# Kernel tuning notes

Measured on AMD Instinct MI355X. Metric: run time of the kernel, lower is better.

The kernel has to match this reference:

```python
import jax, jax.numpy as jnp
import numpy as np

N_ATOMS = 100_000
N_EDGES = 1_600_000
N_RADIAL = 16
N_ELEM = 119          # periodic table size used by per-element scale/shift
HIDDEN = 512
N_FEAT = N_RADIAL + N_RADIAL * N_RADIAL  # M0 + M1-contraction features = 272
R_CUT = 5.0
EPS = 1e-8


def setup_inputs() -> dict:
    key = jax.random.key(0)
    ks = jax.random.split(key, 10)
    R = jax.random.normal(ks[0], (N_ATOMS, 3), jnp.float32)
    Z = jax.random.randint(ks[1], (N_ATOMS,), 0, N_ELEM).astype(jnp.int32)
    idx = jax.random.randint(ks[2], (2, N_EDGES), 0, N_ATOMS)
    box = jnp.zeros((3, 3), jnp.float32)
    offsets = jnp.zeros((N_EDGES, 3), jnp.float32)
    # descriptor params: Gaussian radial basis centers / width
    centers = jnp.linspace(0.0, R_CUT, N_RADIAL, dtype=jnp.float32)
    width = jnp.asarray(0.5, jnp.float32)
    # readout MLP params
    W1 = jax.random.normal(ks[3], (N_FEAT, HIDDEN), jnp.float32) / np.sqrt(N_FEAT)
    b1 = jnp.zeros((HIDDEN,), jnp.float32)
    W2 = jax.random.normal(ks[4], (HIDDEN, HIDDEN), jnp.float32) / np.sqrt(HIDDEN)
    b2 = jnp.zeros((HIDDEN,), jnp.float32)
    W3 = jax.random.normal(ks[5], (HIDDEN, 1), jnp.float32) / np.sqrt(HIDDEN)
    b3 = jnp.zeros((1,), jnp.float32)
    # per-element scale/shift
    scale = jnp.ones((N_ELEM,), jnp.float32)
    shift = jax.random.normal(ks[6], (N_ELEM,), jnp.float32)
    return {"R": R, "Z": Z, "idx": idx, "box": box, "offsets": offsets,
            "centers": centers, "width": width,
            "W1": W1, "b1": b1, "W2": W2, "b2": b2, "W3": W3, "b3": b3,
            "scale": scale, "shift": shift}


def reference(R, Z, idx, box, offsets, centers, width,
              W1, b1, W2, b2, W3, b3, scale, shift):
    n = R.shape[0]
    idx_i, idx_j = idx[0], idx[1]
    # edge gather + free displacement (init_box == 0): dr = displacement(Rj, Ri) = Rj - Ri
    dr = R[idx_j] - R[idx_i]                      # (E, 3)
    r = jnp.linalg.norm(dr, axis=-1, keepdims=True)  # (E, 1)
    d = dr / (r + EPS)                            # unit directions (E, 3)
    # Gaussian radial basis (E, K)
    b = jnp.exp(-((r - centers[None, :]) ** 2) / (2.0 * width * width))
    # scatter-sum moments per atom
    M0 = jax.ops.segment_sum(b, idx_i, num_segments=n)                       # (N, K)
    M1 = jax.ops.segment_sum(b[:, :, None] * d[:, None, :], idx_i,
                             num_segments=n)                                 # (N, K, 3)
    # rotation-invariant gaussian-moment contraction
    G1 = jnp.einsum('nad,nbd->nab', M1, M1).reshape(n, -1)                   # (N, K*K)
    feat = jnp.concatenate([M0, G1], axis=-1)                                # (N, 272)
    # per-atom readout MLP (swish)
    h = jax.nn.silu(feat @ W1 + b1)
    h = jax.nn.silu(h @ W2 + b2)
    h = h @ W3 + b3                                                          # (N, 1)
    # per-element scale/shift, then total energy
    atomic_energies = scale[Z][:, None] * h + shift[Z][:, None]
    return jnp.sum(atomic_energies)
```

## Files before the change

kernel.cpp:

```cpp
#include <hip/hip_runtime.h>
#include <hip/hip_bf16.h>
#include <cstdint>

#define HID 512
#define K1P 288

typedef __attribute__((ext_vector_type(8))) short bf16x8;
typedef __attribute__((ext_vector_type(4))) float f32x4;

__device__ __forceinline__ short f2bf(float x) {
    __hip_bfloat16 h = __float2bfloat16(x);
    return *(short*)&h;
}
__device__ __forceinline__ float silu(float x) {
    return x * (1.0f / (1.0f + __expf(-x)));
}
__device__ __forceinline__ void gl_lds16(const void* src, void* dst) {
    __builtin_amdgcn_global_load_lds(
        (const __attribute__((address_space(1))) void*)src,
        (__attribute__((address_space(3))) void*)dst, 16, 0, 0);
}
__device__ __forceinline__ int xcd_swz(int bid, int nwg) {
    int q = nwg >> 3, r = nwg & 7;
    int xcd = bid & 7, i = bid >> 3;
    int base = (xcd < r) ? xcd * (q + 1) : r * (q + 1) + (xcd - r) * q;
    return base + i;
}

__global__ __launch_bounds__(256) void hist_kernel(
    const int* __restrict__ idx, int* __restrict__ counts, int nEdges)
{
    int e = blockIdx.x * 256 + threadIdx.x;
    if (e < nEdges) atomicAdd(&counts[idx[e]], 1);
}

__global__ __launch_bounds__(1024) void scan1_kernel(
    const int* __restrict__ counts, int* __restrict__ starts,
    int* __restrict__ blockSum, int n)
{
    __shared__ int wsum[16];
    int t = threadIdx.x, lane = t & 63, wid = t >> 6;
    int i = blockIdx.x * 1024 + t;
    int v = (i < n) ? counts[i] : 0;
    int incl = v;
    #pragma unroll
    for (int off = 1; off < 64; off <<= 1) {
        int u = __shfl_up(incl, off);
        if (lane >= off) incl += u;
    }
    if (lane == 63) wsum[wid] = incl;
    __syncthreads();
    if (t < 16) {
        int s = wsum[t];
        #pragma unroll
        for (int off = 1; off < 16; off <<= 1) {
            int u = __shfl_up(s, off);
            if (t >= off) s += u;
        }
        wsum[t] = s;
    }
    __syncthreads();
    int woff = (wid == 0) ? 0 : wsum[wid - 1];
    if (i < n) starts[i] = woff + incl - v;
    if (t == 0) blockSum[blockIdx.x] = wsum[15];
}

__global__ __launch_bounds__(1024) void scan2_kernel(
    const int* __restrict__ blockSum, int* __restrict__ blockOff,
    int* __restrict__ starts, int nb, int n)
{
    __shared__ int arr[1024];
    int t = threadIdx.x;
    int v = (t < nb) ? blockSum[t] : 0;
    arr[t] = v;
    __syncthreads();
    #pragma unroll
    for (int off = 1; off < 1024; off <<= 1) {
        int x = (t >= off) ? arr[t - off] : 0;
        __syncthreads();
        arr[t] += x;
        __syncthreads();
    }
    if (t < nb) blockOff[t] = arr[t] - v;
    if (t == 0) starts[n] = arr[nb - 1];
}

__global__ __launch_bounds__(1024) void scan3_kernel(
    int* __restrict__ starts, int* __restrict__ cursor,
    const int* __restrict__ blockOff, int n)
{
    int i = blockIdx.x * 1024 + threadIdx.x;
    if (i < n) {
        int s = starts[i] + blockOff[blockIdx.x];
        starts[i] = s;
        cursor[i] = s;
    }
}

__global__ __launch_bounds__(256) void scatter_kernel(
    const float* __restrict__ R, const int* __restrict__ idx,
    int* __restrict__ cursor, float4* __restrict__ sorted, int nEdges)
{
    int e = blockIdx.x * 256 + threadIdx.x;
    if (e >= nEdges) return;
    int i = idx[e];
    int j = idx[nEdges + e];
    float rix = R[3*(size_t)i], riy = R[3*(size_t)i+1], riz = R[3*(size_t)i+2];
    float rjx = R[3*(size_t)j], rjy = R[3*(size_t)j+1], rjz = R[3*(size_t)j+2];
    float dx = rjx - rix, dy = rjy - riy, dz = rjz - riz;
    float r = sqrtf(dx*dx + dy*dy + dz*dz);
    float inv = 1.0f / (r + 1e-8f);
    int pos = atomicAdd(&cursor[i], 1);
    sorted[pos] = make_float4(r, dx*inv, dy*inv, dz*inv);
}

__global__ __launch_bounds__(256) void accum_kernel(
    const float4* __restrict__ sorted, const int* __restrict__ starts,
    const float* __restrict__ centers, const float* __restrict__ width,
    float* __restrict__ M0M1, short* __restrict__ feat16,
    int nAtoms, int useFeat)
{
    __shared__ float sm[4][64];
    int wv = threadIdx.x >> 6, lane = threadIdx.x & 63;
    int atom = blockIdx.x * 4 + wv;
    if (atom >= nAtoms) return;
    int s = starts[atom], e = starts[atom + 1];
    int k = lane >> 2, c = lane & 3;
    float ck = centers[k];
    float w = width[0];
    float inv2w2 = 1.0f / (2.0f * w * w);
    float acc = 0.0f;
    auto term = [&](float4 v) {
        float diff = v.x - ck;
        float b = __expf(-diff * diff * inv2w2);
        float comp = (c == 0) ? 1.0f : ((c == 1) ? v.y : ((c == 2) ? v.z : v.w));
        return b * comp;
    };
    int p = s;
    for (; p + 3 < e; p += 4) {
        float4 v0 = sorted[p];
        float4 v1 = sorted[p + 1];
        float4 v2 = sorted[p + 2];
        float4 v3 = sorted[p + 3];
        acc += term(v0); acc += term(v1); acc += term(v2); acc += term(v3);
    }
    for (; p < e; ++p) acc += term(sorted[p]);

    if (!useFeat) {
        M0M1[(size_t)atom * 64 + lane] = acc;
        return;
    }
    sm[wv][lane] = acc;
    asm volatile("s_waitcnt lgkmcnt(0)" ::: "memory");
    short* frow = feat16 + (size_t)atom * K1P;
    #pragma unroll
    for (int q = 0; q < 5; ++q) {
        int idx5 = q * 64 + lane;
        if (idx5 >= K1P) break;
        float val;
        if (idx5 < 16) {
            val = sm[wv][4 * idx5];
        } else if (idx5 < 272) {
            int g = idx5 - 16, a = g >> 4, b = g & 15;
            val = sm[wv][4*a+1] * sm[wv][4*b+1]
                + sm[wv][4*a+2] * sm[wv][4*b+2]
                + sm[wv][4*a+3] * sm[wv][4*b+3];
        } else {
            val = 0.0f;
        }
        frow[idx5] = f2bf(val);
    }
}

__global__ __launch_bounds__(256) void convW_kernel(
    const float* __restrict__ W, short* __restrict__ Wt, int K, int Kpad, int N)
{
    int n = blockIdx.x * 256 + threadIdx.x;
    int k = blockIdx.y;
    if (n >= N) return;
    float v = (k < K) ? W[(size_t)k * N + n] : 0.0f;
    Wt[(size_t)n * Kpad + k] = f2bf(v);
}

__global__ __launch_bounds__(256, 2) void gemm1_mfma(
    const float* __restrict__ M0M1, const short* __restrict__ W1t,
    const float* __restrict__ bias, short* __restrict__ C, int M, int nwg)
{
    __shared__ float MsT[64][128];
    __shared__ short Asl[2][4096];
    __shared__ short Bsl[4][4096];
    int t = threadIdx.x;
    int w = t >> 6, lane = t & 63;
    int wr = w >> 1, wc = w & 1;
    int li = lane & 15, lg = lane >> 4;
    int lin = xcd_swz(blockIdx.x, nwg);
    int row0 = (lin >> 2) * 128;
    int col0 = (lin & 3) * 128;

    {
        int mrow = t >> 1, mo = (t & 1) * 32;
        int gm = row0 + mrow; if (gm > M - 1) gm = M - 1;
        const float4* src = (const float4*)(M0M1 + (size_t)gm * 64 + mo);
        #pragma unroll
        for (int q = 0; q < 8; ++q) {
            float4 v = src[q];
            int c0 = mo + q * 4;
            MsT[c0+0][mrow] = v.x; MsT[c0+1][mrow] = v.y;
            MsT[c0+2][mrow] = v.z; MsT[c0+3][mrow] = v.w;
        }
    }
    __syncthreads();

    auto stageA = [&](int kt, int buf) {
        #pragma unroll
        for (int p = 0; p < 2; ++p) {
            int cell = p * 256 + t;
            int k8 = cell >> 7, row = cell & 127;
            int kbase = kt * 32 + k8 * 8;
            bf16x8 v;
            if (kbase < 16) {
                #pragma unroll
                for (int j = 0; j < 8; ++j) v[j] = f2bf(MsT[4*(kbase+j)][row]);
            } else if (kbase < 272) {
                int g = kbase - 16, a = g >> 4, b0 = g & 15;
                float ax = MsT[4*a+1][row], ay = MsT[4*a+2][row], az = MsT[4*a+3][row];
                #pragma unroll
                for (int j = 0; j < 8; ++j) {
                    int b = b0 + j;
                    v[j] = f2bf(ax*MsT[4*b+1][row] + ay*MsT[4*b+2][row] + az*MsT[4*b+3][row]);
                }
            } else {
                #pragma unroll
                for (int j = 0; j < 8; ++j) v[j] = 0;
            }
            *(bf16x8*)&Asl[buf][cell * 8] = v;
        }
    };
    auto stageB = [&](int kt, int buf) {
        #pragma unroll
        for (int p = 0; p < 2; ++p) {
            int cell = p * 256 + t;
            int k8 = cell >> 7, col = cell & 127;
            const short* src = W1t + (size_t)(col0 + col) * K1P + kt*32 + k8*8;
            gl_lds16(src, &Bsl[buf][(p * 256 + w * 64) * 8]);
        }
    };

    f32x4 acc[4][4] = {};
    const int NS = K1P / 32;
    stageA(0, 0);
    stageB(0, 0); stageB(1, 1); stageB(2, 2);

    #pragma unroll
    for (int s = 0; s < NS; ++s) {
        if (s <= NS - 3)      asm volatile("s_waitcnt vmcnt(4) lgkmcnt(0)\n\ts_barrier" ::: "memory");
        else if (s == NS - 2) asm volatile("s_waitcnt vmcnt(2) lgkmcnt(0)\n\ts_barrier" ::: "memory");
        else                  asm volatile("s_waitcnt vmcnt(0) lgkmcnt(0)\n\ts_barrier" ::: "memory");
        if (s + 3 < NS) stageB(s + 3, (s + 3) & 3);
        bf16x8 af[4], bfr[4];
        #pragma unroll
        for (int m = 0; m < 4; ++m)
            af[m] = *(const bf16x8*)&Asl[s & 1][(lg*128 + wr*64 + m*16 + li) * 8];
        #pragma unroll
        for (int n = 0; n < 4; ++n)
            bfr[n] = *(const bf16x8*)&Bsl[s & 3][(lg*128 + wc*64 + n*16 + li) * 8];
        if (s + 1 < NS) stageA(s + 1, (s + 1) & 1);
        __builtin_amdgcn_s_setprio(1);
        #pragma unroll
        for (int m = 0; m < 4; ++m)
            #pragma unroll
            for (int n = 0; n < 4; ++n)
                acc[m][n] = __builtin_amdgcn_mfma_f32_16x16x32_bf16(af[m], bfr[n], acc[m][n], 0, 0, 0);
        __builtin_amdgcn_s_setprio(0);
    }

    float bv[4];
    #pragma unroll
    for (int n = 0; n < 4; ++n) bv[n] = bias[col0 + wc*64 + n*16 + li];
    #pragma unroll
    for (int m = 0; m < 4; ++m)
        #pragma unroll
        for (int r = 0; r < 4; ++r) {
            int row = row0 + wr*64 + m*16 + lg*4 + r;
            if (row >= M) continue;
            size_t base = (size_t)row * HID + col0 + wc*64 + li;
            #pragma unroll
            for (int n = 0; n < 4; ++n) {
                float cx = acc[m][n][r] + bv[n];
                C[base + n*16] = f2bf(silu(cx));
            }
        }
}

__global__ __launch_bounds__(256, 3) void gemm_feat(
    const short* __restrict__ F, const short* __restrict__ W1t,
    const float* __restrict__ bias, short* __restrict__ C, int M, int nwg)
{
    __shared__ short Asl[3][4096];
    __shared__ short Bsl[3][4096];
    int t = threadIdx.x;
    int w = t >> 6, lane = t & 63;
    int wr = w >> 1, wc = w & 1;
    int li = lane & 15, lg = lane >> 4;
    int lin = xcd_swz(blockIdx.x, nwg);
    int row0 = (lin >> 2) * 128;
    int col0 = (lin & 3) * 128;

    int rr = t & 127, k8h = t >> 7;
    int grA = row0 + rr; if (grA > M - 1) grA = M - 1;
    const short* aSrc0 = F + (size_t)grA * K1P + k8h * 8;
    const short* aSrc1 = aSrc0 + 16;
    const short* bSrc0 = W1t + (size_t)(col0 + rr) * K1P + k8h * 8;
    const short* bSrc1 = bSrc0 + 16;

    auto stage = [&](int kt, int buf) {
        gl_lds16(aSrc0 + kt * 32, &Asl[buf][(w * 64) * 8]);
        gl_lds16(aSrc1 + kt * 32, &Asl[buf][(256 + w * 64) * 8]);
        gl_lds16(bSrc0 + kt * 32, &Bsl[buf][(w * 64) * 8]);
        gl_lds16(bSrc1 + kt * 32, &Bsl[buf][(256 + w * 64) * 8]);
    };

    f32x4 acc[4][4] = {};
    const int NS = K1P / 32;
    stage(0, 0); stage(1, 1);

    #pragma unroll
    for (int s = 0; s < NS; ++s) {
        if (s < NS - 1) asm volatile("s_waitcnt vmcnt(4)\n\ts_barrier" ::: "memory");
        else            asm volatile("s_waitcnt vmcnt(0)\n\ts_barrier" ::: "memory");
        if (s + 2 < NS) stage(s + 2, (s + 2) % 3);
        bf16x8 af[4], bfr[4];
        #pragma unroll
        for (int m = 0; m < 4; ++m)
            af[m] = *(const bf16x8*)&Asl[s % 3][(lg*128 + wr*64 + m*16 + li) * 8];
        #pragma unroll
        for (int n = 0; n < 4; ++n)
            bfr[n] = *(const bf16x8*)&Bsl[s % 3][(lg*128 + wc*64 + n*16 + li) * 8];
        __builtin_amdgcn_s_setprio(1);
        #pragma unroll
        for (int m = 0; m < 4; ++m)
            #pragma unroll
            for (int n = 0; n < 4; ++n)
                acc[m][n] = __builtin_amdgcn_mfma_f32_16x16x32_bf16(af[m], bfr[n], acc[m][n], 0, 0, 0);
        __builtin_amdgcn_s_setprio(0);
    }

    float bv[4];
    #pragma unroll
    for (int n = 0; n < 4; ++n) bv[n] = bias[col0 + wc*64 + n*16 + li];
    #pragma unroll
    for (int m = 0; m < 4; ++m)
        #pragma unroll
        for (int r = 0; r < 4; ++r) {
            int row = row0 + wr*64 + m*16 + lg*4 + r;
            if (row >= M) continue;
            size_t base = (size_t)row * HID + col0 + wc*64 + li;
            #pragma unroll
            for (int n = 0; n < 4; ++n) {
                float cx = acc[m][n][r] + bv[n];
                C[base + n*16] = f2bf(silu(cx));
            }
        }
}

__global__ __launch_bounds__(256, 3) void gemm2_mfma(
    const short* __restrict__ A, const short* __restrict__ W2t,
    const float* __restrict__ bias, const float* __restrict__ W3,
    const float* __restrict__ b3, const float* __restrict__ scale,
    const float* __restrict__ shift, const int* __restrict__ Z,
    float* __restrict__ out, int M, int nwg)
{
    __shared__ short Asl[3][4096];
    __shared__ short Bsl[3][4096];
    __shared__ float rsum[2][128];
    __shared__ float red[4];
    int t = threadIdx.x;
    int w = t >> 6, lane = t & 63;
    int wr = w >> 1, wc = w & 1;
    int li = lane & 15, lg = lane >> 4;
    int lin = xcd_swz(blockIdx.x, nwg);
    int row0 = (lin >> 2) * 128;
    int col0 = (lin & 3) * 128;

    int rr = t & 127, k8h = t >> 7;
    int grA = row0 + rr; if (grA > M - 1) grA = M - 1;
    const short* aSrc0 = A + (size_t)grA * HID + k8h * 8;
    const short* aSrc1 = aSrc0 + 16;
    const short* bSrc0 = W2t + (size_t)(col0 + rr) * HID + k8h * 8;
    const short* bSrc1 = bSrc0 + 16;

    auto stage = [&](int kt, int buf) {
        gl_lds16(aSrc0 + kt * 32, &Asl[buf][(w * 64) * 8]);
        gl_lds16(aSrc1 + kt * 32, &Asl[buf][(256 + w * 64) * 8]);
        gl_lds16(bSrc0 + kt * 32, &Bsl[buf][(w * 64) * 8]);
        gl_lds16(bSrc1 + kt * 32, &Bsl[buf][(256 + w * 64) * 8]);
    };

    f32x4 acc[4][4] = {};
    const int NS = HID / 32;
    stage(0, 0); stage(1, 1);

    for (int s = 0; s < NS; ++s) {
        if (s < NS - 1) asm volatile("s_waitcnt vmcnt(4)\n\ts_barrier" ::: "memory");
        else            asm volatile("s_waitcnt vmcnt(0)\n\ts_barrier" ::: "memory");
        if (s + 2 < NS) stage(s + 2, (s + 2) % 3);
        bf16x8 af[4], bfr[4];
        #pragma unroll
        for (int m = 0; m < 4; ++m)
            af[m] = *(const bf16x8*)&Asl[s % 3][(lg*128 + wr*64 + m*16 + li) * 8];
        #pragma unroll
        for (int n = 0; n < 4; ++n)
            bfr[n] = *(const bf16x8*)&Bsl[s % 3][(lg*128 + wc*64 + n*16 + li) * 8];
        __builtin_amdgcn_s_setprio(1);
        #pragma unroll
        for (int m = 0; m < 4; ++m)
            #pragma unroll
            for (int n = 0; n < 4; ++n)
                acc[m][n] = __builtin_amdgcn_mfma_f32_16x16x32_bf16(af[m], bfr[n], acc[m][n], 0, 0, 0);
        __builtin_amdgcn_s_setprio(0);
    }

    float bv[4], w3v[4];
    #pragma unroll
    for (int n = 0; n < 4; ++n) {
        int col = col0 + wc*64 + n*16 + li;
        bv[n]  = bias[col];
        w3v[n] = W3[col];
    }
    #pragma unroll
    for (int m = 0; m < 4; ++m)
        #pragma unroll
        for (int r = 0; r < 4; ++r) {
            float s = 0.f;
            #pragma unroll
            for (int n = 0; n < 4; ++n) {
                float cx = acc[m][n][r] + bv[n];
                s += silu(cx) * w3v[n];
            }
            #pragma unroll
            for (int off = 1; off < 16; off <<= 1) s += __shfl_xor(s, off);
            if (li == 0) rsum[wc][wr*64 + m*16 + lg*4 + r] = s;
        }
    __syncthreads();
    float e = 0.f;
    if (t < 128) {
        int row = row0 + t;
        if (row < M) {
            float v = rsum[0][t] + rsum[1][t];
            int z = Z[row];
            e = scale[z] * v;
            if ((lin & 3) == 0) e += scale[z] * b3[0] + shift[z];
        }
    }
    #pragma unroll
    for (int off = 32; off > 0; off >>= 1) e += __shfl_down(e, off);
    if (lane == 0) red[w] = e;
    __syncthreads();
    if (t == 0) atomicAdd(out, red[0] + red[1] + red[2] + red[3]);
}

extern "C" void kernel_launch(void* const* d_in, const int* in_sizes, int n_in,
                              void* d_out, int out_size, void* d_ws, size_t ws_size,
                              hipStream_t stream)
{
    const float* R       = (const float*)d_in[0];
    const int*   Z       = (const int*)  d_in[1];
    const int*   idx     = (const int*)  d_in[2];
    const float* centers = (const float*)d_in[5];
    const float* width   = (const float*)d_in[6];
    const float* W1      = (const float*)d_in[7];
    const float* b1      = (const float*)d_in[8];
    const float* W2      = (const float*)d_in[9];
    const float* b2      = (const float*)d_in[10];
    const float* W3      = (const float*)d_in[11];
    const float* b3      = (const float*)d_in[12];
    const float* scale   = (const float*)d_in[13];
    const float* shift   = (const float*)d_in[14];

    int nAtoms = in_sizes[0] / 3;
    int nEdges = in_sizes[2] / 2;

    size_t m0m1_b = (size_t)nAtoms * 64 * sizeof(float);
    size_t h1_b   = (size_t)nAtoms * HID * 2;
    size_t w1t_b  = (size_t)HID * K1P * 2;
    size_t w2t_b  = (size_t)HID * HID * 2;
    size_t feat_b = (size_t)nAtoms * K1P * 2;
    if (ws_size < m0m1_b + h1_b + w1t_b + w2t_b) return;
    int useFeat = (ws_size >= m0m1_b + h1_b + w1t_b + w2t_b + feat_b) ? 1 : 0;

    char* ws = (char*)d_ws;
    float* M0M1  = (float*)ws;
    char*  regB  = ws + m0m1_b;
    short* h1    = (short*)regB;
    short* W1t   = (short*)(ws + m0m1_b + h1_b);
    short* W2t   = W1t + (size_t)HID * K1P;
    short* feat16 = (short*)(ws + m0m1_b + h1_b + w1t_b + w2t_b);

    int nb = (nAtoms + 1023) / 1024;
    size_t sorted_b = (size_t)nEdges * sizeof(float4);
    float4* sorted = (float4*)regB;
    int* counts   = (int*)(regB + sorted_b);
    int* starts   = counts + nAtoms;
    int* cursor   = starts + nAtoms + 1;
    int* blockSum = cursor + nAtoms;
    int* blockOff = blockSum + nb;
    if (sorted_b + (size_t)(3 * nAtoms + 1 + 2 * nb) * sizeof(int) > h1_b) return;

    float* out = (float*)d_out;

    hipMemsetAsync(counts, 0, (size_t)nAtoms * sizeof(int), stream);
    hipMemsetAsync(out, 0, sizeof(float), stream);

    convW_kernel<<<dim3(2, K1P), 256, 0, stream>>>(W1, W1t, 272, K1P, HID);
    convW_kernel<<<dim3(2, HID), 256, 0, stream>>>(W2, W2t, HID, HID, HID);

    int eb = (nEdges + 255) / 256;
    hist_kernel <<<eb, 256, 0, stream>>>(idx, counts, nEdges);
    scan1_kernel<<<nb, 1024, 0, stream>>>(counts, starts, blockSum, nAtoms);
    scan2_kernel<<<1, 1024, 0, stream>>>(blockSum, blockOff, starts, nb, nAtoms);
    scan3_kernel<<<nb, 1024, 0, stream>>>(starts, cursor, blockOff, nAtoms);
    scatter_kernel<<<eb, 256, 0, stream>>>(R, idx, cursor, sorted, nEdges);
    accum_kernel<<<(nAtoms + 3) / 4, 256, 0, stream>>>(sorted, starts, centers, width,
                                                       M0M1, feat16, nAtoms, useFeat);

    int gb = (nAtoms + 127) / 128;
    int nwg = gb * 4;
    if (useFeat)
        gemm_feat<<<nwg, 256, 0, stream>>>(feat16, W1t, b1, h1, nAtoms, nwg);
    else
        gemm1_mfma<<<nwg, 256, 0, stream>>>(M0M1, W1t, b1, h1, nAtoms, nwg);
    gemm2_mfma<<<nwg, 256, 0, stream>>>(h1, W2t, b2, W3, b3, scale, shift, Z, out, nAtoms, nwg);
}
```

Measured before the change: 435.9 us.

## Widen GEMM tiles to 128x256 with 512-thread blocks for MLP layers

Both MLP GEMM kernels now use 512-thread blocks (8 waves in a 2x4 layout) that each compute a 128x256 output tile instead of 128x128. Each A tile is loaded once per block and reused across twice as many output columns, which halves A-side global/LDS traffic and halves the number of workgroups. The cost is more LDS per block, fewer blocks resident per CU, and fewer blocks overall, which may reduce occupancy and latency hiding. The final reduction in the second GEMM is widened to four column groups.

```diff
diff --git a/kernel.cpp b/kernel.cpp
--- a/kernel.cpp
+++ b/kernel.cpp
@@ -292,32 +292,34 @@
         }
 }
 
-__global__ __launch_bounds__(256, 3) void gemm_feat(
+__global__ __launch_bounds__(512) void gemm_feat(
     const short* __restrict__ F, const short* __restrict__ W1t,
     const float* __restrict__ bias, short* __restrict__ C, int M, int nwg)
 {
     __shared__ short Asl[3][4096];
-    __shared__ short Bsl[3][4096];
+    __shared__ short Bsl[3][8192];
     int t = threadIdx.x;
     int w = t >> 6, lane = t & 63;
-    int wr = w >> 1, wc = w & 1;
+    int wr = w >> 2, wc = w & 3;
     int li = lane & 15, lg = lane >> 4;
     int lin = xcd_swz(blockIdx.x, nwg);
-    int row0 = (lin >> 2) * 128;
-    int col0 = (lin & 3) * 128;
-
-    int rr = t & 127, k8h = t >> 7;
-    int grA = row0 + rr; if (grA > M - 1) grA = M - 1;
-    const short* aSrc0 = F + (size_t)grA * K1P + k8h * 8;
-    const short* aSrc1 = aSrc0 + 16;
-    const short* bSrc0 = W1t + (size_t)(col0 + rr) * K1P + k8h * 8;
-    const short* bSrc1 = bSrc0 + 16;
+    int row0 = (lin >> 1) * 128;
+    int colB = (lin & 1) * 256;
+
+    int k8A = t >> 7, rowA = t & 127;
+    int grA = row0 + rowA; if (grA > M - 1) grA = M - 1;
+    const short* aSrc = F + (size_t)grA * K1P + k8A * 8;
+    int cellB = t;
+    int k8B0 = cellB >> 8, colB0 = cellB & 255;
+    const short* bSrc0 = W1t + (size_t)(colB + colB0) * K1P + k8B0 * 8;
+    int cellB1 = 512 + t;
+    int k8B1 = cellB1 >> 8, colB1 = cellB1 & 255;
+    const short* bSrc1 = W1t + (size_t)(colB + colB1) * K1P + k8B1 * 8;
 
     auto stage = [&](int kt, int buf) {
-        gl_lds16(aSrc0 + kt * 32, &Asl[buf][(w * 64) * 8]);
-        gl_lds16(aSrc1 + kt * 32, &Asl[buf][(256 + w * 64) * 8]);
+        gl_lds16(aSrc + kt * 32, &Asl[buf][(w * 64) * 8]);
         gl_lds16(bSrc0 + kt * 32, &Bsl[buf][(w * 64) * 8]);
-        gl_lds16(bSrc1 + kt * 32, &Bsl[buf][(256 + w * 64) * 8]);
+        gl_lds16(bSrc1 + kt * 32, &Bsl[buf][(512 + w * 64) * 8]);
     };
 
     f32x4 acc[4][4] = {};
@@ -326,7 +328,7 @@
 
     #pragma unroll
     for (int s = 0; s < NS; ++s) {
-        if (s < NS - 1) asm volatile("s_waitcnt vmcnt(4)\n\ts_barrier" ::: "memory");
+        if (s < NS - 1) asm volatile("s_waitcnt vmcnt(3)\n\ts_barrier" ::: "memory");
         else            asm volatile("s_waitcnt vmcnt(0)\n\ts_barrier" ::: "memory");
         if (s + 2 < NS) stage(s + 2, (s + 2) % 3);
         bf16x8 af[4], bfr[4];
@@ -335,7 +337,7 @@
             af[m] = *(const bf16x8*)&Asl[s % 3][(lg*128 + wr*64 + m*16 + li) * 8];
         #pragma unroll
         for (int n = 0; n < 4; ++n)
-            bfr[n] = *(const bf16x8*)&Bsl[s % 3][(lg*128 + wc*64 + n*16 + li) * 8];
+            bfr[n] = *(const bf16x8*)&Bsl[s % 3][(lg*256 + wc*64 + n*16 + li) * 8];
         __builtin_amdgcn_s_setprio(1);
         #pragma unroll
         for (int m = 0; m < 4; ++m)
@@ -347,14 +349,14 @@
 
     float bv[4];
     #pragma unroll
-    for (int n = 0; n < 4; ++n) bv[n] = bias[col0 + wc*64 + n*16 + li];
+    for (int n = 0; n < 4; ++n) bv[n] = bias[colB + wc*64 + n*16 + li];
     #pragma unroll
     for (int m = 0; m < 4; ++m)
         #pragma unroll
         for (int r = 0; r < 4; ++r) {
             int row = row0 + wr*64 + m*16 + lg*4 + r;
             if (row >= M) continue;
-            size_t base = (size_t)row * HID + col0 + wc*64 + li;
+            size_t base = (size_t)row * HID + colB + wc*64 + li;
             #pragma unroll
             for (int n = 0; n < 4; ++n) {
                 float cx = acc[m][n][r] + bv[n];
@@ -363,7 +365,7 @@
         }
 }
 
-__global__ __launch_bounds__(256, 3) void gemm2_mfma(
+__global__ __launch_bounds__(512) void gemm2_mfma(
     const short* __restrict__ A, const short* __restrict__ W2t,
     const float* __restrict__ bias, const float* __restrict__ W3,
     const float* __restrict__ b3, const float* __restrict__ scale,
@@ -371,29 +373,31 @@
     float* __restrict__ out, int M, int nwg)
 {
     __shared__ short Asl[3][4096];
-    __shared__ short Bsl[3][4096];
-    __shared__ float rsum[2][128];
-    __shared__ float red[4];
+    __shared__ short Bsl[3][8192];
+    __shared__ float rsum[4][128];
+    __shared__ float red[8];
     int t = threadIdx.x;
     int w = t >> 6, lane = t & 63;
-    int wr = w >> 1, wc = w & 1;
+    int wr = w >> 2, wc = w & 3;
     int li = lane & 15, lg = lane >> 4;
     int lin = xcd_swz(blockIdx.x, nwg);
-    int row0 = (lin >> 2) * 128;
-    int col0 = (lin & 3) * 128;
-
-    int rr = t & 127, k8h = t >> 7;
-    int grA = row0 + rr; if (grA > M - 1) grA = M - 1;
-    const short* aSrc0 = A + (size_t)grA * HID + k8h * 8;
-    const short* aSrc1 = aSrc0 + 16;
-    const short* bSrc0 = W2t + (size_t)(col0 + rr) * HID + k8h * 8;
-    const short* bSrc1 = bSrc0 + 16;
+    int row0 = (lin >> 1) * 128;
+    int colB = (lin & 1) * 256;
+
+    int k8A = t >> 7, rowA = t & 127;
+    int grA = row0 + rowA; if (grA > M - 1) grA = M - 1;
+    const short* aSrc = A + (size_t)grA * HID + k8A * 8;
+    int cellB = t;
+    int k8B0 = cellB >> 8, colB0 = cellB & 255;
+    const short* bSrc0 = W2t + (size_t)(colB + colB0) * HID + k8B0 * 8;
+    int cellB1 = 512 + t;
+    int k8B1 = cellB1 >> 8, colB1 = cellB1 & 255;
+    const short* bSrc1 = W2t + (size_t)(colB + colB1) * HID + k8B1 * 8;
 
     auto stage = [&](int kt, int buf) {
-        gl_lds16(aSrc0 + kt * 32, &Asl[buf][(w * 64) * 8]);
-        gl_lds16(aSrc1 + kt * 32, &Asl[buf][(256 + w * 64) * 8]);
+        gl_lds16(aSrc + kt * 32, &Asl[buf][(w * 64) * 8]);
         gl_lds16(bSrc0 + kt * 32, &Bsl[buf][(w * 64) * 8]);
-        gl_lds16(bSrc1 + kt * 32, &Bsl[buf][(256 + w * 64) * 8]);
+        gl_lds16(bSrc1 + kt * 32, &Bsl[buf][(512 + w * 64) * 8]);
     };
 
     f32x4 acc[4][4] = {};
@@ -401,7 +405,7 @@
     stage(0, 0); stage(1, 1);
 
     for (int s = 0; s < NS; ++s) {
-        if (s < NS - 1) asm volatile("s_waitcnt vmcnt(4)\n\ts_barrier" ::: "memory");
+        if (s < NS - 1) asm volatile("s_waitcnt vmcnt(3)\n\ts_barrier" ::: "memory");
         else            asm volatile("s_waitcnt vmcnt(0)\n\ts_barrier" ::: "memory");
         if (s + 2 < NS) stage(s + 2, (s + 2) % 3);
         bf16x8 af[4], bfr[4];
@@ -410,7 +414,7 @@
             af[m] = *(const bf16x8*)&Asl[s % 3][(lg*128 + wr*64 + m*16 + li) * 8];
         #pragma unroll
         for (int n = 0; n < 4; ++n)
-            bfr[n] = *(const bf16x8*)&Bsl[s % 3][(lg*128 + wc*64 + n*16 + li) * 8];
+            bfr[n] = *(const bf16x8*)&Bsl[s % 3][(lg*256 + wc*64 + n*16 + li) * 8];
         __builtin_amdgcn_s_setprio(1);
         #pragma unroll
         for (int m = 0; m < 4; ++m)
@@ -423,7 +427,7 @@
     float bv[4], w3v[4];
     #pragma unroll
     for (int n = 0; n < 4; ++n) {
-        int col = col0 + wc*64 + n*16 + li;
+        int col = colB + wc*64 + n*16 + li;
         bv[n]  = bias[col];
         w3v[n] = W3[col];
     }
@@ -446,17 +450,20 @@
     if (t < 128) {
         int row = row0 + t;
         if (row < M) {
-            float v = rsum[0][t] + rsum[1][t];
+            float v = rsum[0][t] + rsum[1][t] + rsum[2][t] + rsum[3][t];
             int z = Z[row];
             e = scale[z] * v;
-            if ((lin & 3) == 0) e += scale[z] * b3[0] + shift[z];
+            if ((lin & 1) == 0) e += scale[z] * b3[0] + shift[z];
         }
     }
     #pragma unroll
     for (int off = 32; off > 0; off >>= 1) e += __shfl_down(e, off);
     if (lane == 0) red[w] = e;
     __syncthreads();
-    if (t == 0) atomicAdd(out, red[0] + red[1] + red[2] + red[3]);
+    if (t == 0) {
+        float s2 = red[0] + red[1] + red[2] + red[3] + red[4] + red[5] + red[6] + red[7];
+        atomicAdd(out, s2);
+    }
 }
 
 extern "C" void kernel_launch(void* const* d_in, const int* in_sizes, int n_in,
@@ -524,10 +531,14 @@
                                                        M0M1, feat16, nAtoms, useFeat);
 
     int gb = (nAtoms + 127) / 128;
-    int nwg = gb * 4;
-    if (useFeat)
-        gemm_feat<<<nwg, 256, 0, stream>>>(feat16, W1t, b1, h1, nAtoms, nwg);
-    else
+    if (useFeat) {
+        int nwg = gb * 2;
+        gemm_feat<<<nwg, 512, 0, stream>>>(feat16, W1t, b1, h1, nAtoms, nwg);
+        gemm2_mfma<<<nwg, 512, 0, stream>>>(h1, W2t, b2, W3, b3, scale, shift, Z, out, nAtoms, nwg);
+    } else {
+        int nwg = gb * 4;
         gemm1_mfma<<<nwg, 256, 0, stream>>>(M0M1, W1t, b1, h1, nAtoms, nwg);
-    gemm2_mfma<<<nwg, 256, 0, stream>>>(h1, W2t, b2, W3, b3, scale, shift, Z, out, nAtoms, nwg);
-}
+        int nwg2 = gb * 2;
+        gemm2_mfma<<<nwg2, 512, 0, stream>>>(h1, W2t, b2, W3, b3, scale, shift, Z, out, nAtoms, nwg2);
+    }
+}
```

Result: slower. 488.2 us (+12.0%).

## Exploit symmetry of moment contraction to halve first-layer GEMM K dimension

Applied to the files above, without the earlier changes.

The G1 features are symmetric in (a,b), so only the 136 upper-triangular products are stored, and the matching W1 rows are pre-summed (W[a,b]+W[b,a]) into a new folded weight matrix. The feature row and first GEMM K dimension shrink from 288 to 160, cutting feature write/read traffic and MFMA work in gemm_feat. The cost is an extra weight-folding kernel, a small loop-based triangular index decode per feature element, and slightly different bf16 rounding because the weights are summed before conversion.

```diff
diff --git a/kernel.cpp b/kernel.cpp
--- a/kernel.cpp
+++ b/kernel.cpp
@@ -4,6 +4,7 @@
 
 #define HID 512
 #define K1P 288
+#define K1F 160
 
 typedef __attribute__((ext_vector_type(8))) short bf16x8;
 typedef __attribute__((ext_vector_type(4))) float f32x4;
@@ -25,6 +26,11 @@
     int xcd = bid & 7, i = bid >> 3;
     int base = (xcd < r) ? xcd * (q + 1) : r * (q + 1) + (xcd - r) * q;
     return base + i;
+}
+__device__ __forceinline__ void tri_ab(int g, int& a, int& b) {
+    int aa = 0, rem = g;
+    while (rem >= 16 - aa) { rem -= 16 - aa; ++aa; }
+    a = aa; b = aa + rem;
 }
 
 __global__ __launch_bounds__(256) void hist_kernel(
@@ -152,16 +158,17 @@
     }
     sm[wv][lane] = acc;
     asm volatile("s_waitcnt lgkmcnt(0)" ::: "memory");
-    short* frow = feat16 + (size_t)atom * K1P;
-    #pragma unroll
-    for (int q = 0; q < 5; ++q) {
+    short* frow = feat16 + (size_t)atom * K1F;
+    #pragma unroll
+    for (int q = 0; q < 3; ++q) {
         int idx5 = q * 64 + lane;
-        if (idx5 >= K1P) break;
+        if (idx5 >= K1F) break;
         float val;
         if (idx5 < 16) {
             val = sm[wv][4 * idx5];
-        } else if (idx5 < 272) {
-            int g = idx5 - 16, a = g >> 4, b = g & 15;
+        } else if (idx5 < 152) {
+            int a, b;
+            tri_ab(idx5 - 16, a, b);
             val = sm[wv][4*a+1] * sm[wv][4*b+1]
                 + sm[wv][4*a+2] * sm[wv][4*b+2]
                 + sm[wv][4*a+3] * sm[wv][4*b+3];
@@ -180,6 +187,26 @@
     if (n >= N) return;
     float v = (k < K) ? W[(size_t)k * N + n] : 0.0f;
     Wt[(size_t)n * Kpad + k] = f2bf(v);
+}
+
+__global__ __launch_bounds__(256) void convW1f_kernel(
+    const float* __restrict__ W, short* __restrict__ Wf, int N)
+{
+    int n = blockIdx.x * 256 + threadIdx.x;
+    int k = blockIdx.y;
+    if (n >= N) return;
+    float v;
+    if (k < 16) {
+        v = W[(size_t)k * N + n];
+    } else if (k < 152) {
+        int a, b;
+        tri_ab(k - 16, a, b);
+        v = W[(size_t)(16 + a*16 + b) * N + n];
+        if (b > a) v += W[(size_t)(16 + b*16 + a) * N + n];
+    } else {
+        v = 0.0f;
+    }
+    Wf[(size_t)n * K1F + k] = f2bf(v);
 }
 
 __global__ __launch_bounds__(256, 2) void gemm1_mfma(
@@ -293,7 +320,7 @@
 }
 
 __global__ __launch_bounds__(256, 3) void gemm_feat(
-    const short* __restrict__ F, const short* __restrict__ W1t,
+    const short* __restrict__ F, const short* __restrict__ W1f,
     const float* __restrict__ bias, short* __restrict__ C, int M, int nwg)
 {
     __shared__ short Asl[3][4096];
@@ -308,9 +335,9 @@
 
     int rr = t & 127, k8h = t >> 7;
     int grA = row0 + rr; if (grA > M - 1) grA = M - 1;
-    const short* aSrc0 = F + (size_t)grA * K1P + k8h * 8;
+    const short* aSrc0 = F + (size_t)grA * K1F + k8h * 8;
     const short* aSrc1 = aSrc0 + 16;
-    const short* bSrc0 = W1t + (size_t)(col0 + rr) * K1P + k8h * 8;
+    const short* bSrc0 = W1f + (size_t)(col0 + rr) * K1F + k8h * 8;
     const short* bSrc1 = bSrc0 + 16;
 
     auto stage = [&](int kt, int buf) {
@@ -321,7 +348,7 @@
     };
 
     f32x4 acc[4][4] = {};
-    const int NS = K1P / 32;
+    const int NS = K1F / 32;
     stage(0, 0); stage(1, 1);
 
     #pragma unroll
@@ -484,9 +511,10 @@
     size_t h1_b   = (size_t)nAtoms * HID * 2;
     size_t w1t_b  = (size_t)HID * K1P * 2;
     size_t w2t_b  = (size_t)HID * HID * 2;
-    size_t feat_b = (size_t)nAtoms * K1P * 2;
+    size_t w1f_b  = (size_t)HID * K1F * 2;
+    size_t feat_b = (size_t)nAtoms * K1F * 2;
     if (ws_size < m0m1_b + h1_b + w1t_b + w2t_b) return;
-    int useFeat = (ws_size >= m0m1_b + h1_b + w1t_b + w2t_b + feat_b) ? 1 : 0;
+    int useFeat = (ws_size >= m0m1_b + h1_b + w1t_b + w2t_b + w1f_b + feat_b) ? 1 : 0;
 
     char* ws = (char*)d_ws;
     float* M0M1  = (float*)ws;
@@ -494,7 +522,8 @@
     short* h1    = (short*)regB;
     short* W1t   = (short*)(ws + m0m1_b + h1_b);
     short* W2t   = W1t + (size_t)HID * K1P;
-    short* feat16 = (short*)(ws + m0m1_b + h1_b + w1t_b + w2t_b);
+    short* W1f   = W2t + (size_t)HID * HID;
+    short* feat16 = (short*)(ws + m0m1_b + h1_b + w1t_b + w2t_b + w1f_b);
 
     int nb = (nAtoms + 1023) / 1024;
     size_t sorted_b = (size_t)nEdges * sizeof(float4);
@@ -513,6 +542,8 @@
 
     convW_kernel<<<dim3(2, K1P), 256, 0, stream>>>(W1, W1t, 272, K1P, HID);
     convW_kernel<<<dim3(2, HID), 256, 0, stream>>>(W2, W2t, HID, HID, HID);
+    if (useFeat)
+        convW1f_kernel<<<dim3(2, K1F), 256, 0, stream>>>(W1, W1f, HID);
 
     int eb = (nEdges + 255) / 256;
     hist_kernel <<<eb, 256, 0, stream>>>(idx, counts, nEdges);
@@ -526,7 +557,7 @@
     int gb = (nAtoms + 127) / 128;
     int nwg = gb * 4;
     if (useFeat)
-        gemm_feat<<<nwg, 256, 0, stream>>>(feat16, W1t, b1, h1, nAtoms, nwg);
+        gemm_feat<<<nwg, 256, 0, stream>>>(feat16, W1f, b1, h1, nAtoms, nwg);
     else
         gemm1_mfma<<<nwg, 256, 0, stream>>>(M0M1, W1t, b1, h1, nAtoms, nwg);
     gemm2_mfma<<<nwg, 256, 0, stream>>>(h1, W2t, b2, W3, b3, scale, shift, Z, out, nAtoms, nwg);
```

Measured after the change: 426.7 us. -2.1%, faster.
